# Kernel tuning notes

Hardware: AMD Instinct MI355X
Metric: run time of the kernel (lower is better)

Reference implementation:

```python
import jax, jax.numpy as jnp
import numpy as np
import math

B, S, D, H, HD, M, E = 4, 1024, 1024, 16, 64, 4096, 1024
EPS = 1e-6

def rms_norm(x, w):
    # torch: x / (||x||/sqrt(d) + eps) * w  (eps added to the norm, not norm^2)
    n = jnp.sqrt(jnp.sum(x * x, axis=-1, keepdims=True)) / math.sqrt(x.shape[-1])
    return x / (n + EPS) * w

def rope(x):
    # x: (B,H,S,hd)
    hd, s = x.shape[-1], x.shape[2]
    inv = 1.0 / (10000.0 ** (jnp.arange(0, hd, 2, dtype=jnp.float32) / hd))
    fr = jnp.arange(s, dtype=jnp.float32)[:, None] * inv[None, :]        # (S, hd/2)
    emb = jnp.concatenate([fr, fr], axis=-1)                              # (S, hd)
    cos, sin = jnp.cos(emb), jnp.sin(emb)
    x1, x2 = x[..., : hd // 2], x[..., hd // 2 :]
    rot = jnp.concatenate([-x2, x1], axis=-1)
    return x * cos + rot * sin

def setup_inputs() -> dict:
    key = jax.random.key(0)
    ks = jax.random.split(key, 18)
    p = lambda k, sh: jax.random.normal(k, sh, jnp.float32) * 0.02
    return {
        'x': jax.random.normal(ks[0], (B, S, D), jnp.float32),
        'emb': jax.random.normal(ks[1], (B, E), jnp.float32),
        'ln1_w': jnp.ones((D,), jnp.float32),
        'ln1_lW': p(ks[2], (E, 2 * D)), 'ln1_lb': p(ks[3], (2 * D,)),
        'ln2_w': jnp.ones((D,), jnp.float32),
        'ln2_lW': p(ks[4], (E, 2 * D)), 'ln2_lb': p(ks[5], (2 * D,)),
        'qkv_W': p(ks[6], (D, 3 * D)), 'qkv_b': p(ks[7], (3 * D,)),
        'proj_W': p(ks[8], (D, D)), 'proj_b': p(ks[9], (D,)),
        'nq_w': jnp.ones((HD,), jnp.float32), 'nk_w': jnp.ones((HD,), jnp.float32),
        'mlp_W': p(ks[10], (D, 2 * M)), 'mlp_b': p(ks[11], (2 * M,)),
        'out_W': p(ks[12], (M, D)), 'out_b': p(ks[13], (D,)),
        'gates_W': p(ks[14], (E, 2 * D)), 'gates_b': p(ks[15], (2 * D,)),
    }

def reference(x, emb, ln1_w, ln1_lW, ln1_lb, ln2_w, ln2_lW, ln2_lb,
              qkv_W, qkv_b, proj_W, proj_b, nq_w, nk_w,
              mlp_W, mlp_b, out_W, out_b, gates_W, gates_b):
    g = emb @ gates_W + gates_b                       # (B, 2D)
    gate_mha, gate_mlp = g[:, :D], g[:, D:]
    # AdaLNZero 1
    ss = emb @ ln1_lW + ln1_lb                        # (B, 2D): [scale | shift]
    xn = rms_norm(x, ln1_w) * (1.0 + ss[:, None, :D]) + ss[:, None, D:]
    # RoPE attention with qk RMSNorm
    qkv = (xn @ qkv_W + qkv_b).reshape(B, S, 3, H, HD).transpose(2, 0, 3, 1, 4)
    q, k, v = qkv[0], qkv[1], qkv[2]                  # each (B,H,S,HD)
    q = rms_norm(rope(q), nq_w)
    k = rms_norm(rope(k), nk_w)
    scores = jnp.einsum('bhqd,bhkd->bhqk', q, k) * (HD ** -0.5)
    attn = jnp.nan_to_num(jax.nn.softmax(scores, axis=-1))
    ao = jnp.einsum('bhqk,bhkd->bhqd', attn, v).transpose(0, 2, 1, 3).reshape(B, S, D)
    x = x + gate_mha[:, None, :] * (ao @ proj_W + proj_b)
    # AdaLNZero 2 + SwiGLU MLP
    ss2 = emb @ ln2_lW + ln2_lb
    xn2 = rms_norm(x, ln2_w) * (1.0 + ss2[:, None, :D]) + ss2[:, None, D:]
    h = xn2 @ mlp_W + mlp_b                           # (B,S,2M)
    act = h[..., :M] * jax.nn.silu(h[..., M:])
    mlp_out = act @ out_W + out_b
    return x + gate_mlp[:, None, :] * mlp_out
```

## Files before the change

### kernel.cpp

```cpp
#include <hip/hip_runtime.h>
#include <hip/hip_bf16.h>
#include <math.h>

#define B_ 4
#define S_ 1024
#define D_ 1024
#define H_ 16
#define HD_ 64
#define M_ 4096
#define E_ 1024

using bf16 = __hip_bfloat16;
typedef short bf16x8 __attribute__((ext_vector_type(8)));
typedef float f32x4 __attribute__((ext_vector_type(4)));

__device__ __forceinline__ void gl_lds16(const void* g, void* l) {
    __builtin_amdgcn_global_load_lds(
        (__attribute__((address_space(1))) void*)(g),
        (__attribute__((address_space(3))) void*)(l), 16, 0, 0);
}



#define STG_A(q, pb, kc) gl_lds16(A  + gAoff[q] + (kc), &sA[pb][(q) * 4096 + tid * 8])
#define STG_B(q, pb, kc) gl_lds16(Bt + gBoff[q] + (kc), &sB[pb][(q) * 4096 + tid * 8])

#define LDA(mh, m, h) (*(const bf16x8*)(cA + aRow + (mh) * 8192 + (m) * 2048 + (h)))
#define LDB(nh, n, h) (*(const bf16x8*)(cB + bRow + (nh) * 4096 + (n) * 2048 + (h)))

#define MFMA_QUAD(MH, NH, BF)                                                             \
    __builtin_amdgcn_s_setprio(1);                                                        \
    _Pragma("unroll")                                                                     \
    for (int m = 0; m < 4; ++m) {                                                         \
        _Pragma("unroll")                                                                 \
        for (int n = 0; n < 2; ++n) {                                                     \
            acc[(MH)*4+m][(NH)*2+n] = __builtin_amdgcn_mfma_f32_16x16x32_bf16(            \
                aF[m][0], BF[n][0], acc[(MH)*4+m][(NH)*2+n], 0, 0, 0);                    \
            acc[(MH)*4+m][(NH)*2+n] = __builtin_amdgcn_mfma_f32_16x16x32_bf16(            \
                aF[m][1], BF[n][1], acc[(MH)*4+m][(NH)*2+n], 0, 0, 0);                    \
        }                                                                                 \
    }                                                                                     \
    __builtin_amdgcn_s_setprio(0);

#define GEMM256_LOOP                                                                      \
    const int nt = K >> 6;                                                                \
    for (int t = 0; t < nt; ++t) {                                                        \
        const int pb = t & 1;                                                             \
        const char* cA = (const char*)sA[pb];                                             \
        const char* cB = (const char*)sB[pb];                                             \
        const int kc2 = (t + 2) << 6;                                                     \
        const bool pf = (t + 2) < nt;                                                     \
        bf16x8 aF[4][2], b0F[2][2], b1F[2][2];                                            \
                                          \
        _Pragma("unroll")                                                                 \
        for (int m = 0; m < 4; ++m) {                                                     \
            aF[m][0] = LDA(0, m, cs0);                                                    \
            aF[m][1] = LDA(0, m, cs1);                                                    \
        }                                                                                 \
        _Pragma("unroll")                                                                 \
        for (int n = 0; n < 2; ++n) {                                                     \
            b0F[n][0] = LDB(0, n, cs0);                                                   \
            b0F[n][1] = LDB(0, n, cs1);                                                   \
        }                                                                                 \
        __builtin_amdgcn_s_barrier();                                                     \
        MFMA_QUAD(0, 0, b0F)                                                              \
        __builtin_amdgcn_s_barrier();                                                     \
                         \
        _Pragma("unroll")                                                                 \
        for (int n = 0; n < 2; ++n) {                                                     \
            b1F[n][0] = LDB(1, n, cs0);                                                   \
            b1F[n][1] = LDB(1, n, cs1);                                                   \
        }                                                                                 \
        if (pf) { STG_A(0, pb, kc2); STG_A(2, pb, kc2); }                                 \
        __builtin_amdgcn_s_barrier();                                                     \
        MFMA_QUAD(0, 1, b1F)                                                              \
        __builtin_amdgcn_s_barrier();                                                     \
                               \
        _Pragma("unroll")                                                                 \
        for (int m = 0; m < 4; ++m) {                                                     \
            aF[m][0] = LDA(1, m, cs0);                                                    \
            aF[m][1] = LDA(1, m, cs1);                                                    \
        }                                                                                 \
        if (pf) { STG_B(0, pb, kc2); STG_B(1, pb, kc2);                                   \
                  STG_B(2, pb, kc2); STG_B(3, pb, kc2); }                                 \
        __builtin_amdgcn_s_barrier();                                                     \
        MFMA_QUAD(1, 1, b1F)                                                              \
        __builtin_amdgcn_s_barrier();                                                     \
                                 \
        if (pf) { STG_A(1, pb, kc2); STG_A(3, pb, kc2); }                                 \
        __builtin_amdgcn_s_barrier();                                                     \
        MFMA_QUAD(1, 0, b0F)                                                              \
        if (pf)              { asm volatile("s_waitcnt vmcnt(8)" ::: "memory"); }         \
        else if (t + 1 < nt) { asm volatile("s_waitcnt vmcnt(0)" ::: "memory"); }         \
        __builtin_amdgcn_s_barrier();                                                     \
    }

__global__ __launch_bounds__(256) void transpose_kernel(
    const float* __restrict__ W, bf16* __restrict__ Wt, int K, int N)
{
    __shared__ float tile[32][33];
    int n0 = blockIdx.x * 32, k0 = blockIdx.y * 32;
    int tx = threadIdx.x & 31, ty = threadIdx.x >> 5;
    #pragma unroll
    for (int r = ty; r < 32; r += 8)
        tile[r][tx] = W[(long)(k0 + r) * N + n0 + tx];
    __syncthreads();
    #pragma unroll
    for (int r = ty; r < 32; r += 8)
        Wt[(long)(n0 + r) * K + k0 + tx] = __float2bfloat16(tile[tx][r]);
}

__global__ __launch_bounds__(256) void embgemm_kernel(
    const float* __restrict__ emb,
    const float* __restrict__ W0, const float* __restrict__ b0,
    const float* __restrict__ W1, const float* __restrict__ b1,
    const float* __restrict__ W2, const float* __restrict__ b2,
    float* __restrict__ G, float* __restrict__ SS, float* __restrict__ SS2)
{
    __shared__ float se[256];
    int b = blockIdx.y;
    int k0 = blockIdx.z * 256;
    if (threadIdx.x < 256) se[threadIdx.x] = emb[b * 1024 + k0 + threadIdx.x];
    __syncthreads();
    int j = blockIdx.x * 256 + threadIdx.x;
    int which = j >> 11, col = j & 2047;
    const float* W  = which == 0 ? W0 : (which == 1 ? W1 : W2);
    const float* bb = which == 0 ? b0 : (which == 1 ? b1 : b2);
    float acc = (k0 == 0) ? bb[col] : 0.f;
    #pragma unroll 4
    for (int k = 0; k < 256; ++k) acc += se[k] * W[(long)(k0 + k) * 2048 + col];
    float* out = which == 0 ? G : (which == 1 ? SS : SS2);
    atomicAdd(&out[b * 2048 + col], acc);
}

__global__ __launch_bounds__(256) void rmsmod_kernel(
    const float* __restrict__ x, const float* __restrict__ w,
    const float* __restrict__ ss, bf16* __restrict__ out)
{
    int row = blockIdx.x;
    int b = row >> 10;
    const float* xr = x + (long)row * D_;
    float4 v = ((const float4*)xr)[threadIdx.x];
    float ssum = v.x * v.x + v.y * v.y + v.z * v.z + v.w * v.w;
    #pragma unroll
    for (int off = 32; off; off >>= 1) ssum += __shfl_xor(ssum, off);
    __shared__ float red[4];
    if ((threadIdx.x & 63) == 0) red[threadIdx.x >> 6] = ssum;
    __syncthreads();
    float tot = red[0] + red[1] + red[2] + red[3];
    float n = sqrtf(tot) * (1.f / 32.f);
    float inv = 1.f / (n + 1e-6f);
    int d0 = threadIdx.x * 4;
    const float* ssb = ss + b * 2048;
    bf16 t[4];
    t[0] = __float2bfloat16(v.x * inv * w[d0 + 0] * (1.f + ssb[d0 + 0]) + ssb[D_ + d0 + 0]);
    t[1] = __float2bfloat16(v.y * inv * w[d0 + 1] * (1.f + ssb[d0 + 1]) + ssb[D_ + d0 + 1]);
    t[2] = __float2bfloat16(v.z * inv * w[d0 + 2] * (1.f + ssb[d0 + 2]) + ssb[D_ + d0 + 2]);
    t[3] = __float2bfloat16(v.w * inv * w[d0 + 3] * (1.f + ssb[d0 + 3]) + ssb[D_ + d0 + 3]);
    *(uint2*)&out[(long)row * D_ + d0] = *(uint2*)t;
}

__global__ __launch_bounds__(512) void gemm256_kernel(
    const bf16* __restrict__ A, const bf16* __restrict__ Bt,
    const float* __restrict__ bias, bf16* __restrict__ Cb,
    int N, int K)
{
    __shared__ bf16 sA[2][16384];
    __shared__ bf16 sB[2][16384];
    const int tid = threadIdx.x;
    const int wave = tid >> 6, lane = tid & 63;
    const int wr = wave >> 2, wc = wave & 3;
    const int cl = lane & 15, qd = lane >> 4;

    const int num_pid_n = N >> 8;
    const int cpx = gridDim.x >> 3;
    int wg = (blockIdx.x & 7) * cpx + (blockIdx.x >> 3);
    const int group_size = 8 * num_pid_n;
    const int group_id = wg / group_size;
    const int pid_in = wg - group_id * group_size;
    const int m0 = (group_id * 8 + (pid_in & 7)) * 256;
    const int n0 = (pid_in >> 3) * 256;

    long gAoff[4], gBoff[4];
    #pragma unroll
    for (int q = 0; q < 4; ++q) {
        int c = tid + q * 512;
        int cs = c ^ ((c >> 3) & 7);
        int row = cs >> 3, col = (cs & 7) * 8;
        gAoff[q] = (long)(m0 + row) * K + col;
        gBoff[q] = (long)(n0 + row) * K + col;
    }

    #pragma unroll
    for (int q = 0; q < 4; ++q) { STG_A(q, 0, 0); STG_B(q, 0, 0); }
    #pragma unroll
    for (int q = 0; q < 4; ++q) { STG_A(q, 1, 64); STG_B(q, 1, 64); }

    f32x4 acc[8][4] = {};
    const int swz = (cl & 7) << 4;
    const int aRow = (wr * 128 + cl) * 128;
    const int bRow = (wc * 64 + cl) * 128;
    const int cs0 = (qd * 16) ^ swz;
    const int cs1 = (qd * 16 + 64) ^ swz;

    asm volatile("s_waitcnt vmcnt(8)" ::: "memory");
    __builtin_amdgcn_s_barrier();

    GEMM256_LOOP

    #pragma unroll
    for (int m = 0; m < 8; ++m) {
        #pragma unroll
        for (int n = 0; n < 4; ++n) {
            int col = n0 + wc * 64 + n * 16 + cl;
            float bs = bias[col];
            #pragma unroll
            for (int i = 0; i < 4; ++i) {
                int row = m0 + wr * 128 + m * 16 + qd * 4 + i;
                Cb[(long)row * N + col] = __float2bfloat16(acc[m][n][i] + bs);
            }
        }
    }
}

__global__ __launch_bounds__(512) void gemm256_mlp_kernel(
    const bf16* __restrict__ A, const bf16* __restrict__ Bt,
    const float* __restrict__ bias, bf16* __restrict__ ACT, int K)
{
    __shared__ bf16 sA[2][16384];
    __shared__ bf16 sB[2][16384];
    const int tid = threadIdx.x;
    const int wave = tid >> 6, lane = tid & 63;
    const int wr = wave >> 2, wc = wave & 3;
    const int cl = lane & 15, qd = lane >> 4;

    const int num_pid_n = 32;
    const int cpx = gridDim.x >> 3;
    int wg = (blockIdx.x & 7) * cpx + (blockIdx.x >> 3);
    const int group_size = 8 * num_pid_n;
    const int group_id = wg / group_size;
    const int pid_in = wg - group_id * group_size;
    const int m0 = (group_id * 8 + (pid_in & 7)) * 256;
    const int n0 = (pid_in >> 3) * 128;

    long gAoff[4], gBoff[4];
    #pragma unroll
    for (int q = 0; q < 4; ++q) {
        int c = tid + q * 512;
        int cs = c ^ ((c >> 3) & 7);
        int row = cs >> 3, col = (cs & 7) * 8;
        gAoff[q] = (long)(m0 + row) * K + col;
        int pp = row >> 5, hf = (row >> 4) & 1, wi = row & 15;
        gBoff[q] = (long)(hf * 4096 + n0 + pp * 16 + wi) * K + col;
    }

    #pragma unroll
    for (int q = 0; q < 4; ++q) { STG_A(q, 0, 0); STG_B(q, 0, 0); }
    #pragma unroll
    for (int q = 0; q < 4; ++q) { STG_A(q, 1, 64); STG_B(q, 1, 64); }

    f32x4 acc[8][4] = {};
    const int swz = (cl & 7) << 4;
    const int aRow = (wr * 128 + cl) * 128;
    const int bRow = (wc * 64 + cl) * 128;
    const int cs0 = (qd * 16) ^ swz;
    const int cs1 = (qd * 16 + 64) ^ swz;

    asm volatile("s_waitcnt vmcnt(8)" ::: "memory");
    __builtin_amdgcn_s_barrier();

    GEMM256_LOOP

    #pragma unroll
    for (int m = 0; m < 8; ++m) {
        #pragma unroll
        for (int pr = 0; pr < 2; ++pr) {
            int col = n0 + wc * 32 + pr * 16 + cl;
            float bs1 = bias[col];
            float bs2 = bias[4096 + col];
            #pragma unroll
            for (int i = 0; i < 4; ++i) {
                int row = m0 + wr * 128 + m * 16 + qd * 4 + i;
                float h1 = acc[m][pr * 2 + 0][i] + bs1;
                float h2 = acc[m][pr * 2 + 1][i] + bs2;
                float sg = 1.f / (1.f + __expf(-h2));
                ACT[(long)row * 4096 + col] = __float2bfloat16(h1 * h2 * sg);
            }
        }
    }
}

__global__ __launch_bounds__(256) void gemm64_kernel(
    const bf16* __restrict__ A, const bf16* __restrict__ Bt,
    const float* __restrict__ bias,
    bf16* __restrict__ Cb, float* __restrict__ Cf,
    const float* __restrict__ resid, const float* __restrict__ gates, int gate_off,
    int Mrows, int N, int K, int mode)
{
    __shared__ bf16 sA[64 * 32];
    __shared__ bf16 sB[64 * 32];
    const int tid = threadIdx.x;
    const int wave = tid >> 6, lane = tid & 63;
    const int num_pid_n = N >> 6;
    const int pid = blockIdx.x;
    const int group_size = 8 * num_pid_n;
    const int group_id = pid / group_size;
    const int pid_in = pid - group_id * group_size;
    const int pid_m = group_id * 8 + (pid_in & 7);
    const int pid_n = pid_in >> 3;
    const int m0 = pid_m * 64, n0 = pid_n * 64;
    const int wm = (wave & 1) * 32, wn = (wave >> 1) * 32;
    const int cl = lane & 15, qd = lane >> 4;

    f32x4 acc[2][2] = {};

    const int c = tid;
    const int rr = c >> 2, ss = (c & 3) ^ ((c >> 3) & 3);
    const bf16* gA = A + (long)(m0 + rr) * K + ss * 8;
    const bf16* gB = Bt + (long)(n0 + rr) * K + ss * 8;
    bf16* lA = &sA[wave * 512];
    bf16* lB = &sB[wave * 512];

    const int q8s = (qd ^ ((cl >> 1) & 3)) * 8;

    for (int kc = 0; kc < K; kc += 32) {
        gl_lds16(gA + kc, lA);
        gl_lds16(gB + kc, lB);
        __syncthreads();
        bf16x8 af[2], bfr[2];
        #pragma unroll
        for (int t = 0; t < 2; ++t)
            af[t] = *(const bf16x8*)&sA[(wm + cl + t * 16) * 32 + q8s];
        #pragma unroll
        for (int u = 0; u < 2; ++u)
            bfr[u] = *(const bf16x8*)&sB[(wn + cl + u * 16) * 32 + q8s];
        #pragma unroll
        for (int t = 0; t < 2; ++t)
            #pragma unroll
            for (int u = 0; u < 2; ++u)
                acc[t][u] = __builtin_amdgcn_mfma_f32_16x16x32_bf16(af[t], bfr[u], acc[t][u], 0, 0, 0);
        __syncthreads();
    }

    #pragma unroll
    for (int t = 0; t < 2; ++t) {
        #pragma unroll
        for (int u = 0; u < 2; ++u) {
            int col = n0 + wn + u * 16 + cl;
            float bs = bias[col];
            #pragma unroll
            for (int i = 0; i < 4; ++i) {
                int row = m0 + wm + t * 16 + qd * 4 + i;
                float v = acc[t][u][i] + bs;
                if (mode == 0) {
                    Cb[(long)row * N + col] = __float2bfloat16(v);
                } else {
                    int b = row >> 10;
                    float g = gates[b * 2048 + gate_off + col];
                    Cf[(long)row * N + col] = resid[(long)row * N + col] + g * v;
                }
            }
        }
    }
}

__global__ __launch_bounds__(256) void ropenorm_kernel(
    const bf16* __restrict__ qkv, const float* __restrict__ nq_w, const float* __restrict__ nk_w,
    bf16* __restrict__ qh, bf16* __restrict__ kh, bf16* __restrict__ vt)
{
    int gid = blockIdx.x * 4 + (threadIdx.x >> 6);
    int lane = threadIdx.x & 63;
    int b = gid >> 14, s = (gid >> 4) & (S_ - 1), h = gid & (H_ - 1);
    const long base = (long)(b * S_ + s) * 3072 + h * 64 + lane;
    float qv = __bfloat162float(qkv[base]);
    float kv = __bfloat162float(qkv[base + 1024]);
    float vv = __bfloat162float(qkv[base + 2048]);
    int j = lane & 31;
    float inv = exp2f(-(float)j * (13.287712379549449f / 32.f));
    float ang = (float)s * inv;
    float sn, c;
    sincosf(ang, &sn, &c);
    float pq = __shfl_xor(qv, 32);
    float pk = __shfl_xor(kv, 32);
    float rq = (lane < 32) ? -pq : pq;
    float rk = (lane < 32) ? -pk : pk;
    float qr = qv * c + rq * sn;
    float kr = kv * c + rk * sn;
    float sq = qr * qr, sk = kr * kr;
    #pragma unroll
    for (int off = 32; off; off >>= 1) { sq += __shfl_xor(sq, off); sk += __shfl_xor(sk, off); }
    float nq = sqrtf(sq) * 0.125f;
    float nk = sqrtf(sk) * 0.125f;
    float qo = qr / (nq + 1e-6f) * nq_w[lane];
    float ko = kr / (nk + 1e-6f) * nk_w[lane];
    long hb = ((long)(b * H_ + h) * S_ + s) * 64 + lane;
    qh[hb] = __float2bfloat16(qo);
    kh[hb] = __float2bfloat16(ko);
    vt[((long)(b * H_ + h) * 64 + lane) * S_ + s] = __float2bfloat16(vv);
}

__global__ __launch_bounds__(256) void attn_kernel(
    const bf16* __restrict__ qh, const bf16* __restrict__ kh, const bf16* __restrict__ vt,
    bf16* __restrict__ ao)
{
    const int bh = blockIdx.y;
    const int q0 = blockIdx.x * 64;
    const int tid = threadIdx.x, wave = tid >> 6, lane = tid & 63;
    const int cl = lane & 15, qd = lane >> 4;

    __shared__ bf16 sQ[64 * 72];
    __shared__ bf16 sK[64 * 72];
    __shared__ bf16 sV[64 * 72];
    __shared__ bf16 sP[4][16 * 72];

    {
        const bf16* Qg = qh + (long)bh * S_ * 64 + (long)q0 * 64;
        int a = tid, b2 = tid + 256;
        *(uint4*)&sQ[(a >> 3) * 72 + (a & 7) * 8]  = *(const uint4*)&Qg[(a >> 3) * 64 + (a & 7) * 8];
        *(uint4*)&sQ[(b2 >> 3) * 72 + (b2 & 7) * 8] = *(const uint4*)&Qg[(b2 >> 3) * 64 + (b2 & 7) * 8];
    }

    float l_i[4] = {0.f, 0.f, 0.f, 0.f};
    f32x4 o_acc[4] = {};

    const bf16* Kg = kh + (long)bh * S_ * 64;
    const bf16* Vg = vt + (long)bh * 64 * S_;

    for (int kv0 = 0; kv0 < S_; kv0 += 64) {
        __syncthreads();
        {
            int a = tid, b2 = tid + 256;
            *(uint4*)&sK[(a >> 3) * 72 + (a & 7) * 8]   = *(const uint4*)&Kg[((long)kv0 + (a >> 3)) * 64 + (a & 7) * 8];
            *(uint4*)&sK[(b2 >> 3) * 72 + (b2 & 7) * 8] = *(const uint4*)&Kg[((long)kv0 + (b2 >> 3)) * 64 + (b2 & 7) * 8];
            *(uint4*)&sV[(a >> 3) * 72 + (a & 7) * 8]   = *(const uint4*)&Vg[(long)(a >> 3) * S_ + kv0 + (a & 7) * 8];
            *(uint4*)&sV[(b2 >> 3) * 72 + (b2 & 7) * 8] = *(const uint4*)&Vg[(long)(b2 >> 3) * S_ + kv0 + (b2 & 7) * 8];
        }
        __syncthreads();

        f32x4 sfr[4] = {};
        #pragma unroll
        for (int u = 0; u < 4; ++u) {
            #pragma unroll
            for (int ks = 0; ks < 2; ++ks) {
                bf16x8 aq = *(const bf16x8*)&sQ[(wave * 16 + cl) * 72 + ks * 32 + qd * 8];
                bf16x8 bk = *(const bf16x8*)&sK[(u * 16 + cl) * 72 + ks * 32 + qd * 8];
                sfr[u] = __builtin_amdgcn_mfma_f32_16x16x32_bf16(aq, bk, sfr[u], 0, 0, 0);
            }
        }

        #pragma unroll
        for (int i = 0; i < 4; ++i) {
            float sum = 0.f;
            #pragma unroll
            for (int u = 0; u < 4; ++u) {
                float p = __expf(sfr[u][i] * 0.125f - 8.f);
                sum += p;
                sP[wave][(qd * 4 + i) * 72 + u * 16 + cl] = __float2bfloat16(p);
            }
            sum += __shfl_xor(sum, 1);
            sum += __shfl_xor(sum, 2);
            sum += __shfl_xor(sum, 4);
            sum += __shfl_xor(sum, 8);
            l_i[i] += sum;
        }

        #pragma unroll
        for (int ks = 0; ks < 2; ++ks) {
            bf16x8 ap = *(const bf16x8*)&sP[wave][cl * 72 + ks * 32 + qd * 8];
            #pragma unroll
            for (int u = 0; u < 4; ++u) {
                bf16x8 bv = *(const bf16x8*)&sV[(u * 16 + cl) * 72 + ks * 32 + qd * 8];
                o_acc[u] = __builtin_amdgcn_mfma_f32_16x16x32_bf16(ap, bv, o_acc[u], 0, 0, 0);
            }
        }
    }

    #pragma unroll
    for (int i = 0; i < 4; ++i) {
        float invl = 1.f / l_i[i];
        int row = q0 + wave * 16 + qd * 4 + i;
        #pragma unroll
        for (int u = 0; u < 4; ++u) {
            int d = u * 16 + cl;
            ao[((long)(bh >> 4) * S_ + row) * D_ + (bh & 15) * 64 + d] =
                __float2bfloat16(o_acc[u][i] * invl);
        }
    }
}

extern "C" void kernel_launch(void* const* d_in, const int* in_sizes, int n_in,
                              void* d_out, int out_size, void* d_ws, size_t ws_size,
                              hipStream_t stream) {
    const float* x       = (const float*)d_in[0];
    const float* emb     = (const float*)d_in[1];
    const float* ln1_w   = (const float*)d_in[2];
    const float* ln1_lW  = (const float*)d_in[3];
    const float* ln1_lb  = (const float*)d_in[4];
    const float* ln2_w   = (const float*)d_in[5];
    const float* ln2_lW  = (const float*)d_in[6];
    const float* ln2_lb  = (const float*)d_in[7];
    const float* qkv_W   = (const float*)d_in[8];
    const float* qkv_b   = (const float*)d_in[9];
    const float* proj_W  = (const float*)d_in[10];
    const float* proj_b  = (const float*)d_in[11];
    const float* nq_w    = (const float*)d_in[12];
    const float* nk_w    = (const float*)d_in[13];
    const float* mlp_W   = (const float*)d_in[14];
    const float* mlp_b   = (const float*)d_in[15];
    const float* out_W   = (const float*)d_in[16];
    const float* out_b   = (const float*)d_in[17];
    const float* gates_W = (const float*)d_in[18];
    const float* gates_b = (const float*)d_in[19];
    float* out = (float*)d_out;

    char* p = (char*)d_ws;
    if (ws_size < 159481856UL) return;
    bf16* WT_QKV  = (bf16*)p;  p += 6291456;
    bf16* WT_PROJ = (bf16*)p;  p += 2097152;
    bf16* WT_MLP  = (bf16*)p;  p += 16777216;
    bf16* WT_OUT  = (bf16*)p;  p += 8388608;
    float* G      = (float*)p; p += 32768;
    float* SSb    = (float*)p; p += 32768;
    float* SS2b   = (float*)p; p += 32768;
    float* X1     = (float*)p; p += 16777216;
    bf16* XN2     = (bf16*)p;  p += 8388608;
    bf16* ACT     = (bf16*)p;  p += 33554432;
    char* REG = p;
    bf16* XN   = (bf16*)(REG);
    bf16* QKV  = (bf16*)(REG + 8388608);
    bf16* QH   = (bf16*)(REG + 33554432);
    bf16* KH   = (bf16*)(REG + 41943040);
    bf16* VT   = (bf16*)(REG + 50331648);
    bf16* AO   = (bf16*)(REG + 58720256);

    dim3 blk(256);
    hipMemsetAsync(G, 0, 98304, stream);
    transpose_kernel<<<dim3(96, 32),  blk, 0, stream>>>(qkv_W,  WT_QKV, 1024, 3072);
    transpose_kernel<<<dim3(32, 32),  blk, 0, stream>>>(proj_W, WT_PROJ, 1024, 1024);
    transpose_kernel<<<dim3(256, 32), blk, 0, stream>>>(mlp_W,  WT_MLP, 1024, 8192);
    transpose_kernel<<<dim3(32, 128), blk, 0, stream>>>(out_W,  WT_OUT, 4096, 1024);
    embgemm_kernel<<<dim3(24, 4, 4), blk, 0, stream>>>(emb, gates_W, gates_b, ln1_lW, ln1_lb,
                                                       ln2_lW, ln2_lb, G, SSb, SS2b);
    rmsmod_kernel<<<dim3(4096), blk, 0, stream>>>(x, ln1_w, SSb, XN);
    gemm256_kernel<<<dim3(192), dim3(512), 0, stream>>>(XN, WT_QKV, qkv_b, QKV, 3072, 1024);
    ropenorm_kernel<<<dim3(16384), blk, 0, stream>>>(QKV, nq_w, nk_w, QH, KH, VT);
    attn_kernel<<<dim3(16, 64), blk, 0, stream>>>(QH, KH, VT, AO);
    gemm64_kernel<<<dim3(1024), blk, 0, stream>>>(AO, WT_PROJ, proj_b, nullptr, X1,
                                                  x, G, 0, 4096, 1024, 1024, 1);
    rmsmod_kernel<<<dim3(4096), blk, 0, stream>>>(X1, ln2_w, SS2b, XN2);
    gemm256_mlp_kernel<<<dim3(512), dim3(512), 0, stream>>>(XN2, WT_MLP, mlp_b, ACT, 1024);
    gemm64_kernel<<<dim3(1024), blk, 0, stream>>>(ACT, WT_OUT, out_b, nullptr, out,
                                                  X1, G, 1024, 4096, 1024, 4096, 1);
}
```

Measured before the change: 498.9 us.

## Replace out-projection GEMM with split-K 256x128 tiled kernel plus fused epilogue

The final MLP down-projection (K=4096, N=1024) moves from the small 64x64 tile kernel to a new 256x128 tile, 512-thread MFMA kernel. It splits K in two so 256 workgroups fill the device, writes fp32 partials, and adds them in a separate elementwise kernel that also applies bias, gate and residual. The goal is more data reuse per tile and better MFMA use, paid for by extra fp32 partial traffic and one more launch. The existing gemm256 main loop also gains explicit lgkmcnt(0) waits before each MFMA quad.

Measured after the change: 480.8 us. 3.6% less time.

```diff
diff --git a/kernel.cpp b/kernel.cpp
--- a/kernel.cpp
+++ b/kernel.cpp
@@ -63,6 +63,7 @@
             b0F[n][1] = LDB(0, n, cs1);                                                   \
         }                                                                                 \
         __builtin_amdgcn_s_barrier();                                                     \
+        asm volatile("s_waitcnt lgkmcnt(0)" ::: "memory");                                \
         MFMA_QUAD(0, 0, b0F)                                                              \
         __builtin_amdgcn_s_barrier();                                                     \
                          \
@@ -73,6 +74,7 @@
         }                                                                                 \
         if (pf) { STG_A(0, pb, kc2); STG_A(2, pb, kc2); }                                 \
         __builtin_amdgcn_s_barrier();                                                     \
+        asm volatile("s_waitcnt lgkmcnt(0)" ::: "memory");                                \
         MFMA_QUAD(0, 1, b1F)                                                              \
         __builtin_amdgcn_s_barrier();                                                     \
                                \
@@ -84,11 +86,13 @@
         if (pf) { STG_B(0, pb, kc2); STG_B(1, pb, kc2);                                   \
                   STG_B(2, pb, kc2); STG_B(3, pb, kc2); }                                 \
         __builtin_amdgcn_s_barrier();                                                     \
+        asm volatile("s_waitcnt lgkmcnt(0)" ::: "memory");                                \
         MFMA_QUAD(1, 1, b1F)                                                              \
         __builtin_amdgcn_s_barrier();                                                     \
                                  \
         if (pf) { STG_A(1, pb, kc2); STG_A(3, pb, kc2); }                                 \
         __builtin_amdgcn_s_barrier();                                                     \
+        asm volatile("s_waitcnt lgkmcnt(0)" ::: "memory");                                \
         MFMA_QUAD(1, 0, b0F)                                                              \
         if (pf)              { asm volatile("s_waitcnt vmcnt(8)" ::: "memory"); }         \
         else if (t + 1 < nt) { asm volatile("s_waitcnt vmcnt(0)" ::: "memory"); }         \
@@ -288,6 +292,141 @@
             }
         }
     }
+}
+
+#define MFMA_HQ(MH)                                                                       \
+    __builtin_amdgcn_s_setprio(1);                                                        \
+    _Pragma("unroll")                                                                     \
+    for (int m = 0; m < 4; ++m) {                                                         \
+        _Pragma("unroll")                                                                 \
+        for (int n = 0; n < 2; ++n) {                                                     \
+            acc[(MH)*4+m][n] = __builtin_amdgcn_mfma_f32_16x16x32_bf16(                   \
+                aF[m][0], bF[n][0], acc[(MH)*4+m][n], 0, 0, 0);                           \
+            acc[(MH)*4+m][n] = __builtin_amdgcn_mfma_f32_16x16x32_bf16(                   \
+                aF[m][1], bF[n][1], acc[(MH)*4+m][n], 0, 0, 0);                           \
+        }                                                                                 \
+    }                                                                                     \
+    __builtin_amdgcn_s_setprio(0);
+
+__global__ __launch_bounds__(512) void gemm256x128_kernel(
+    const bf16* __restrict__ A, const bf16* __restrict__ Bt,
+    float* __restrict__ P0, float* __restrict__ P1, int N, int K)
+{
+    __shared__ bf16 sA[2][16384];
+    __shared__ bf16 sB[2][8192];
+    const int tid = threadIdx.x;
+    const int wave = tid >> 6, lane = tid & 63;
+    const int wr = wave >> 2, wc = wave & 3;
+    const int cl = lane & 15, qd = lane >> 4;
+
+    const int cpx = gridDim.x >> 3;
+    int wg = (blockIdx.x & 7) * cpx + (blockIdx.x >> 3);
+    const int split = wg >> 7;
+    const int w2 = wg & 127;
+    const int group_id = w2 >> 6;
+    const int pid_in = w2 & 63;
+    const int m0 = (group_id * 8 + (pid_in & 7)) * 256;
+    const int n0 = (pid_in >> 3) * 128;
+    const int Kh = K >> 1;
+    A  += (long)split * Kh;
+    Bt += (long)split * Kh;
+
+    long gAoff[4], gBoff[2];
+    #pragma unroll
+    for (int q = 0; q < 4; ++q) {
+        int c = tid + q * 512;
+        int cs = c ^ ((c >> 3) & 7);
+        int row = cs >> 3, col = (cs & 7) * 8;
+        gAoff[q] = (long)(m0 + row) * K + col;
+        if (q < 2) gBoff[q] = (long)(n0 + row) * K + col;
+    }
+
+    const int nt = Kh >> 6;
+    STG_A(0, 0, 0); STG_A(2, 0, 0); STG_B(0, 0, 0); STG_B(1, 0, 0);
+    STG_A(1, 0, 0); STG_A(3, 0, 0);
+    if (nt > 1) { STG_A(0, 1, 64); STG_A(2, 1, 64); STG_B(0, 1, 64); STG_B(1, 1, 64); }
+
+    f32x4 acc[8][2] = {};
+    const int swz = (cl & 7) << 4;
+    const int aRow = (wr * 128 + cl) * 128;
+    const int bRow = (wc * 32 + cl) * 128;
+    const int cs0 = (qd * 16) ^ swz;
+    const int cs1 = (qd * 16 + 64) ^ swz;
+
+    if (nt > 1) { asm volatile("s_waitcnt vmcnt(4)" ::: "memory"); }
+    else        { asm volatile("s_waitcnt vmcnt(0)" ::: "memory"); }
+    __builtin_amdgcn_s_barrier();
+
+    for (int t = 0; t < nt; ++t) {
+        const int pb = t & 1;
+        const char* cA = (const char*)sA[pb];
+        const char* cB = (const char*)sB[pb];
+        bf16x8 aF[4][2], bF[2][2];
+        #pragma unroll
+        for (int m = 0; m < 4; ++m) {
+            aF[m][0] = *(const bf16x8*)(cA + aRow + m * 2048 + cs0);
+            aF[m][1] = *(const bf16x8*)(cA + aRow + m * 2048 + cs1);
+        }
+        #pragma unroll
+        for (int n = 0; n < 2; ++n) {
+            bF[n][0] = *(const bf16x8*)(cB + bRow + n * 2048 + cs0);
+            bF[n][1] = *(const bf16x8*)(cB + bRow + n * 2048 + cs1);
+        }
+        if (t + 1 < nt) { STG_A(1, pb ^ 1, (t + 1) << 6); STG_A(3, pb ^ 1, (t + 1) << 6); }
+        __builtin_amdgcn_s_barrier();
+        asm volatile("s_waitcnt lgkmcnt(0)" ::: "memory");
+        MFMA_HQ(0)
+        __builtin_amdgcn_s_barrier();
+        #pragma unroll
+        for (int m = 0; m < 4; ++m) {
+            aF[m][0] = *(const bf16x8*)(cA + aRow + 8192 + m * 2048 + cs0);
+            aF[m][1] = *(const bf16x8*)(cA + aRow + 8192 + m * 2048 + cs1);
+        }
+        if (t + 2 < nt) { STG_A(0, pb, (t + 2) << 6); STG_A(2, pb, (t + 2) << 6);
+                          STG_B(0, pb, (t + 2) << 6); STG_B(1, pb, (t + 2) << 6); }
+        __builtin_amdgcn_s_barrier();
+        asm volatile("s_waitcnt lgkmcnt(0)" ::: "memory");
+        MFMA_HQ(1)
+        if (t + 2 < nt)      { asm volatile("s_waitcnt vmcnt(4)" ::: "memory"); }
+        else if (t + 1 < nt) { asm volatile("s_waitcnt vmcnt(0)" ::: "memory"); }
+        __builtin_amdgcn_s_barrier();
+    }
+
+    float* P = split ? P1 : P0;
+    #pragma unroll
+    for (int m = 0; m < 8; ++m) {
+        #pragma unroll
+        for (int n = 0; n < 2; ++n) {
+            int col = n0 + wc * 32 + n * 16 + cl;
+            #pragma unroll
+            for (int i = 0; i < 4; ++i) {
+                int row = m0 + wr * 128 + m * 16 + qd * 4 + i;
+                P[(long)row * N + col] = acc[m][n][i];
+            }
+        }
+    }
+}
+
+__global__ __launch_bounds__(256) void fuseout_kernel(
+    const float* __restrict__ p0, const float* __restrict__ p1,
+    const float* __restrict__ bias, const float* __restrict__ resid,
+    const float* __restrict__ gates, float* __restrict__ out)
+{
+    int idx = blockIdx.x * 256 + threadIdx.x;
+    int row = idx >> 8;
+    int b = row >> 10;
+    int c4 = (idx & 255) * 4;
+    float4 a = ((const float4*)p0)[idx];
+    float4 c = ((const float4*)p1)[idx];
+    float4 r = ((const float4*)resid)[idx];
+    float4 bb = *(const float4*)&bias[c4];
+    float4 gg = *(const float4*)&gates[b * 2048 + 1024 + c4];
+    float4 o;
+    o.x = r.x + gg.x * (a.x + c.x + bb.x);
+    o.y = r.y + gg.y * (a.y + c.y + bb.y);
+    o.z = r.z + gg.z * (a.z + c.z + bb.z);
+    o.w = r.w + gg.w * (a.w + c.w + bb.w);
+    ((float4*)out)[idx] = o;
 }
 
 __global__ __launch_bounds__(256) void gemm64_kernel(
@@ -532,6 +671,8 @@
     bf16* KH   = (bf16*)(REG + 41943040);
     bf16* VT   = (bf16*)(REG + 50331648);
     bf16* AO   = (bf16*)(REG + 58720256);
+    float* PF0 = (float*)(REG);
+    float* PF1 = (float*)(REG + 16777216);
 
     dim3 blk(256);
     hipMemsetAsync(G, 0, 98304, stream);
@@ -549,6 +690,6 @@
                                                   x, G, 0, 4096, 1024, 1024, 1);
     rmsmod_kernel<<<dim3(4096), blk, 0, stream>>>(X1, ln2_w, SS2b, XN2);
     gemm256_mlp_kernel<<<dim3(512), dim3(512), 0, stream>>>(XN2, WT_MLP, mlp_b, ACT, 1024);
-    gemm64_kernel<<<dim3(1024), blk, 0, stream>>>(ACT, WT_OUT, out_b, nullptr, out,
-                                                  X1, G, 1024, 4096, 1024, 4096, 1);
-}
+    gemm256x128_kernel<<<dim3(256), dim3(512), 0, stream>>>(ACT, WT_OUT, PF0, PF1, 1024, 4096);
+    fuseout_kernel<<<dim3(4096), blk, 0, stream>>>(PF0, PF1, out_b, X1, G, out);
+}
```
